# Optimization experiments

Hardware: AMD Instinct MI355X
Metric: run time of the kernel (lower is better)

Reference implementation:

```python
import jax, jax.numpy as jnp
import numpy as np

N_NODES = 100000
N_EDGES = 1600000
IN_C = 128
HID = 128
LAT = 64
N_LAYERS = 3
N_GRAPHS = 1000


def setup_inputs() -> dict:
    key = jax.random.key(0)
    ks = jax.random.split(key, 16)
    x = jax.random.normal(ks[0], (N_NODES, IN_C), dtype=jnp.float32)
    edge_index = jax.random.randint(ks[1], (2, N_EDGES), 0, N_NODES, dtype=jnp.int64)
    batch = jnp.sort(jax.random.randint(ks[2], (N_NODES,), 0, N_GRAPHS, dtype=jnp.int64))
    s = 1.0 / np.sqrt(HID)
    # per-layer GIN MLP params (in_c == hidden for all layers since IN_C == HID)
    W1 = jax.random.normal(ks[3], (N_LAYERS, IN_C, HID), dtype=jnp.float32) * s
    b1 = jnp.zeros((N_LAYERS, HID), dtype=jnp.float32)
    W2 = jax.random.normal(ks[4], (N_LAYERS, HID, HID), dtype=jnp.float32) * s
    b2 = jnp.zeros((N_LAYERS, HID), dtype=jnp.float32)
    W_mu = jax.random.normal(ks[5], (HID, LAT), dtype=jnp.float32) * s
    b_mu = jnp.zeros((LAT,), dtype=jnp.float32)
    W_lv = jax.random.normal(ks[6], (HID, LAT), dtype=jnp.float32) * s
    b_lv = jnp.zeros((LAT,), dtype=jnp.float32)
    return {"x": x, "edge_index": edge_index, "batch": batch,
            "W1": W1, "b1": b1, "W2": W2, "b2": b2,
            "W_mu": W_mu, "b_mu": b_mu, "W_lv": W_lv, "b_lv": b_lv}


def reference(x, edge_index, batch, W1, b1, W2, b2, W_mu, b_mu, W_lv, b_lv):
    src, dst = edge_index[0], edge_index[1]
    h = x
    for i in range(N_LAYERS):
        # GINConv (eps=0): h' = MLP(h + sum_{j in N(i)} h_j); scatter-add over edges
        agg = h + jax.ops.segment_sum(h[src], dst, num_segments=N_NODES)
        h = jax.nn.relu(agg @ W1[i] + b1[i])
        h = jax.nn.relu(h @ W2[i] + b2[i])
        h = jax.nn.relu(h)  # extra ReLU in forward after conv (idempotent here)
    # global_add_pool: segment-sum nodes into graphs
    g = jax.ops.segment_sum(h, batch, num_segments=N_GRAPHS)  # [G, HID]
    mu = g @ W_mu + b_mu
    logvar = g @ W_lv + b_lv
    return (mu, logvar)
```

## Files before the change

kernel.cpp:

```cpp
#include <hip/hip_runtime.h>

#define N_NODES 100000
#define N_EDGES 1600000
#define HID 128
#define LAT 64
#define N_LAYERS 3
#define N_GRAPHS 1000
#define CAP 64
#define NBIN 391
#define MAXBIN 4608
#define ACHUNK 8192
#define ABLOCKS ((N_EDGES + ACHUNK - 1) / ACHUNK)

typedef short bf16x8 __attribute__((ext_vector_type(8)));
typedef float f32x4 __attribute__((ext_vector_type(4)));

__device__ __forceinline__ float bf2f(unsigned short h) {
    union { unsigned int u; float f; } c;
    c.u = ((unsigned int)h) << 16;
    return c.f;
}
__device__ __forceinline__ unsigned short f2bf(float f) {
    union { float f; unsigned int u; } c;
    c.f = f;
    unsigned int u = c.u;
    return (unsigned short)((u + 0x7fffu + ((u >> 16) & 1u)) >> 16);
}
__device__ __forceinline__ unsigned int pack2(float a, float b) {
    return (unsigned int)f2bf(a) | ((unsigned int)f2bf(b) << 16);
}
__device__ __forceinline__ void addrow(float* acc, uint4 w) {
    acc[0] += bf2f((unsigned short)w.x); acc[1] += bf2f((unsigned short)(w.x >> 16));
    acc[2] += bf2f((unsigned short)w.y); acc[3] += bf2f((unsigned short)(w.y >> 16));
    acc[4] += bf2f((unsigned short)w.z); acc[5] += bf2f((unsigned short)(w.z >> 16));
    acc[6] += bf2f((unsigned short)w.w); acc[7] += bf2f((unsigned short)(w.w >> 16));
}

__global__ __launch_bounds__(256) void cvt_x_kernel(const float* __restrict__ x,
                                                    unsigned short* __restrict__ xb, int n4) {
    int i = blockIdx.x * 256 + threadIdx.x;
    if (i >= n4) return;
    float4 v = ((const float4*)x)[i];
    ((uint2*)xb)[i] = make_uint2(pack2(v.x, v.y), pack2(v.z, v.w));
}

__global__ __launch_bounds__(256) void wt_kernel(const float* __restrict__ W1,
                                                 const float* __restrict__ W2,
                                                 unsigned short* __restrict__ Wt) {
    int m = blockIdx.x;
    const float* W = ((m & 1) ? W2 : W1) + (size_t)(m >> 1) * HID * HID;
    unsigned short* D = Wt + (size_t)m * HID * HID;
    for (int idx = threadIdx.x; idx < HID * HID; idx += 256) {
        int n = idx >> 7, k = idx & 127;
        D[n * HID + k] = f2bf(W[k * HID + n]);
    }
}

__global__ __launch_bounds__(256) void binA_kernel(const int* __restrict__ ei,
                                                   int* __restrict__ gcnt,
                                                   unsigned int* __restrict__ ebin) {
    __shared__ unsigned int scount[NBIN];
    __shared__ unsigned int sfill[NBIN];
    int t = threadIdx.x;
    int base = blockIdx.x * ACHUNK;
    int n = N_EDGES - base;
    if (n > ACHUNK) n = ACHUNK;
    for (int i = t; i < NBIN; i += 256) scount[i] = 0u;
    __syncthreads();
    for (int i = t; i < n; i += 256) {
        int d = ei[N_EDGES + base + i];
        atomicAdd(&scount[d >> 8], 1u);
    }
    __syncthreads();
    for (int b = t; b < NBIN; b += 256) {
        unsigned int c = scount[b];
        sfill[b] = c ? (unsigned int)atomicAdd(&gcnt[b], (int)c) : 0u;
    }
    __syncthreads();
    for (int i = t; i < n; i += 256) {
        int s = ei[base + i];
        int d = ei[N_EDGES + base + i];
        int b = d >> 8;
        unsigned int pos = atomicAdd(&sfill[b], 1u);
        ebin[(size_t)b * MAXBIN + pos] = ((unsigned int)(d & 255) << 24) | (unsigned int)s;
    }
}

__global__ __launch_bounds__(256) void binB_kernel(const unsigned int* __restrict__ ebin,
                                                   const int* __restrict__ gcnt,
                                                   int* __restrict__ cnt,
                                                   int* __restrict__ csr) {
    __shared__ int scnt[256];
    int b = blockIdx.x;
    int t = threadIdx.x;
    scnt[t] = 0;
    __syncthreads();
    int n0 = b << 8;
    int c = gcnt[b];
    const unsigned int* src = ebin + (size_t)b * MAXBIN;
    for (int i = t; i < c; i += 256) {
        unsigned int e = src[i];
        int dl = (int)(e >> 24);
        int slot = atomicAdd(&scnt[dl], 1);
        csr[(size_t)(n0 + dl) * CAP + slot] = (int)(e & 0xFFFFFFu);
    }
    __syncthreads();
    int node = n0 + t;
    if (node < N_NODES) cnt[node] = scnt[t];
}

__global__ __launch_bounds__(256) void gather_kernel(const unsigned short* __restrict__ h,
                                                     const int* __restrict__ cnt,
                                                     const int* __restrict__ csr,
                                                     unsigned short* __restrict__ agg) {
    int t = threadIdx.x;
    int node = blockIdx.x * 16 + (t >> 4);
    int q = t & 15;
    if (node >= N_NODES) return;
    const int* nl = csr + (size_t)node * CAP;
    int deg = cnt[node];
    float acc[8] = {0.f, 0.f, 0.f, 0.f, 0.f, 0.f, 0.f, 0.f};
    addrow(acc, *(const uint4*)(h + (size_t)node * HID + q * 8));
    int e = 0;
    for (; e + 8 <= deg; e += 8) {
        int s0 = nl[e], s1 = nl[e + 1], s2 = nl[e + 2], s3 = nl[e + 3];
        int s4 = nl[e + 4], s5 = nl[e + 5], s6 = nl[e + 6], s7 = nl[e + 7];
        uint4 w0 = *(const uint4*)(h + (size_t)s0 * HID + q * 8);
        uint4 w1 = *(const uint4*)(h + (size_t)s1 * HID + q * 8);
        uint4 w2 = *(const uint4*)(h + (size_t)s2 * HID + q * 8);
        uint4 w3 = *(const uint4*)(h + (size_t)s3 * HID + q * 8);
        uint4 w4 = *(const uint4*)(h + (size_t)s4 * HID + q * 8);
        uint4 w5 = *(const uint4*)(h + (size_t)s5 * HID + q * 8);
        uint4 w6 = *(const uint4*)(h + (size_t)s6 * HID + q * 8);
        uint4 w7 = *(const uint4*)(h + (size_t)s7 * HID + q * 8);
        addrow(acc, w0); addrow(acc, w1); addrow(acc, w2); addrow(acc, w3);
        addrow(acc, w4); addrow(acc, w5); addrow(acc, w6); addrow(acc, w7);
    }
    for (; e + 4 <= deg; e += 4) {
        int s0 = nl[e], s1 = nl[e + 1], s2 = nl[e + 2], s3 = nl[e + 3];
        uint4 w0 = *(const uint4*)(h + (size_t)s0 * HID + q * 8);
        uint4 w1 = *(const uint4*)(h + (size_t)s1 * HID + q * 8);
        uint4 w2 = *(const uint4*)(h + (size_t)s2 * HID + q * 8);
        uint4 w3 = *(const uint4*)(h + (size_t)s3 * HID + q * 8);
        addrow(acc, w0); addrow(acc, w1); addrow(acc, w2); addrow(acc, w3);
    }
    for (; e < deg; ++e) {
        addrow(acc, *(const uint4*)(h + (size_t)nl[e] * HID + q * 8));
    }
    uint4 o;
    o.x = pack2(acc[0], acc[1]);
    o.y = pack2(acc[2], acc[3]);
    o.z = pack2(acc[4], acc[5]);
    o.w = pack2(acc[6], acc[7]);
    *(uint4*)(agg + (size_t)node * HID + q * 8) = o;
}

__global__ __launch_bounds__(256) void mlp_kernel(const unsigned short* __restrict__ A,
                                                  const unsigned short* __restrict__ W1t,
                                                  const float* __restrict__ b1,
                                                  const unsigned short* __restrict__ W2t,
                                                  const float* __restrict__ b2,
                                                  unsigned short* __restrict__ out) {
    __shared__ unsigned short sA[64][136];
    __shared__ unsigned short sW[128][40];
    __shared__ float sb[128];
    const int t = threadIdx.x;
    const int w = t >> 6;
    const int l = t & 63;
    const int lm = l & 15;
    const int quad = l >> 4;
    const int row0 = blockIdx.x * 64;

    for (int idx = t; idx < 1024; idx += 256) {
        int r = idx >> 4, c = idx & 15;
        int grow = row0 + r;
        uint4 v = make_uint4(0u, 0u, 0u, 0u);
        if (grow < N_NODES) v = *(const uint4*)(A + (size_t)grow * HID + c * 8);
        *(uint4*)&sA[r][c * 8] = v;
    }

    const unsigned short* Wt[2] = {W1t, W2t};
    const float* bias[2] = {b1, b2};

    for (int p = 0; p < 2; ++p) {
        if (t < 128) sb[t] = bias[p][t];
        f32x4 acc[8];
#pragma unroll
        for (int nt = 0; nt < 8; ++nt) acc[nt] = (f32x4){0.f, 0.f, 0.f, 0.f};

        for (int kc = 0; kc < 4; ++kc) {
            __syncthreads();
            for (int idx = t; idx < 512; idx += 256) {
                int n = idx >> 2, kq = idx & 3;
                *(uint4*)&sW[n][kq * 8] =
                    *(const uint4*)(Wt[p] + (size_t)n * HID + kc * 32 + kq * 8);
            }
            __syncthreads();
            bf16x8 a = *(const bf16x8*)&sA[w * 16 + lm][kc * 32 + quad * 8];
#pragma unroll
            for (int nt = 0; nt < 8; ++nt) {
                bf16x8 b = *(const bf16x8*)&sW[nt * 16 + lm][quad * 8];
                acc[nt] = __builtin_amdgcn_mfma_f32_16x16x32_bf16(a, b, acc[nt], 0, 0, 0);
            }
        }
        __syncthreads();
#pragma unroll
        for (int nt = 0; nt < 8; ++nt) {
            float bv = sb[nt * 16 + lm];
#pragma unroll
            for (int r = 0; r < 4; ++r) {
                int m = w * 16 + quad * 4 + r;
                float val = fmaxf(acc[nt][r] + bv, 0.f);
                sA[m][nt * 16 + lm] = f2bf(val);
            }
        }
        __syncthreads();
    }
    for (int idx = t; idx < 1024; idx += 256) {
        int r = idx >> 4, c = idx & 15;
        int grow = row0 + r;
        if (grow < N_NODES)
            *(uint4*)(out + (size_t)grow * HID + c * 8) = *(const uint4*)&sA[r][c * 8];
    }
}

__global__ __launch_bounds__(256) void pool_kernel(const unsigned short* __restrict__ h,
                                                   const int* __restrict__ batch,
                                                   float* __restrict__ g) {
    const int S = 16;
    int t = threadIdx.x;
    int grp = t >> 4;
    int q = t & 15;
    int n0 = (blockIdx.x * 16 + grp) * S;
    if (n0 >= N_NODES) return;
    int n1 = n0 + S;
    if (n1 > N_NODES) n1 = N_NODES;
    int cur = batch[n0];
    float acc[8] = {0.f, 0.f, 0.f, 0.f, 0.f, 0.f, 0.f, 0.f};
    for (int n = n0; n < n1; ++n) {
        int b = batch[n];
        if (b != cur) {
            float* gp = g + (size_t)cur * HID + q * 8;
#pragma unroll
            for (int i = 0; i < 8; ++i) { atomicAdd(gp + i, acc[i]); acc[i] = 0.f; }
            cur = b;
        }
        addrow(acc, *(const uint4*)(h + (size_t)n * HID + q * 8));
    }
    float* gp = g + (size_t)cur * HID + q * 8;
#pragma unroll
    for (int i = 0; i < 8; ++i) atomicAdd(gp + i, acc[i]);
}

__global__ __launch_bounds__(128) void head_kernel(const float* __restrict__ g,
                                                   const float* __restrict__ Wmu,
                                                   const float* __restrict__ bmu,
                                                   const float* __restrict__ Wlv,
                                                   const float* __restrict__ blv,
                                                   float* __restrict__ out) {
    __shared__ float sg[HID];
    int gi = blockIdx.x;
    sg[threadIdx.x] = g[(size_t)gi * HID + threadIdx.x];
    __syncthreads();
    int j = threadIdx.x & 63;
    bool is_lv = threadIdx.x >= 64;
    const float* W = is_lv ? Wlv : Wmu;
    float acc = is_lv ? blv[j] : bmu[j];
    for (int k = 0; k < HID; ++k) acc = fmaf(sg[k], W[k * LAT + j], acc);
    out[(is_lv ? (size_t)N_GRAPHS * LAT : 0) + (size_t)gi * LAT + j] = acc;
}

extern "C" void kernel_launch(void* const* d_in, const int* in_sizes, int n_in,
                              void* d_out, int out_size, void* d_ws, size_t ws_size,
                              hipStream_t stream) {
    const float* x     = (const float*)d_in[0];
    const int*   ei    = (const int*)d_in[1];
    const int*   batch = (const int*)d_in[2];
    const float* W1    = (const float*)d_in[3];
    const float* b1    = (const float*)d_in[4];
    const float* W2    = (const float*)d_in[5];
    const float* b2    = (const float*)d_in[6];
    const float* Wmu   = (const float*)d_in[7];
    const float* bmu   = (const float*)d_in[8];
    const float* Wlv   = (const float*)d_in[9];
    const float* blv   = (const float*)d_in[10];
    float* out = (float*)d_out;

    float* g = (float*)d_ws;
    unsigned short* xb   = (unsigned short*)(g + (size_t)N_GRAPHS * HID);
    unsigned short* agg  = xb + (size_t)N_NODES * HID;
    unsigned short* hbuf = agg + (size_t)N_NODES * HID;
    unsigned short* Wt   = hbuf + (size_t)N_NODES * HID;
    int* cnt  = (int*)(Wt + (size_t)6 * HID * HID);
    int* gcnt = cnt + N_NODES;
    int* csr  = gcnt + NBIN + 1;
    unsigned int* ebin = (unsigned int*)(csr + (size_t)N_NODES * CAP);

    hipMemsetAsync(gcnt, 0, (size_t)NBIN * sizeof(int), stream);
    binA_kernel<<<ABLOCKS, 256, 0, stream>>>(ei, gcnt, ebin);
    binB_kernel<<<NBIN, 256, 0, stream>>>(ebin, gcnt, cnt, csr);

    cvt_x_kernel<<<(N_NODES * HID / 4 + 255) / 256, 256, 0, stream>>>(x, xb,
                                                                      N_NODES * HID / 4);
    wt_kernel<<<6, 256, 0, stream>>>(W1, W2, Wt);

    const unsigned short* hcur = xb;
    for (int i = 0; i < N_LAYERS; ++i) {
        gather_kernel<<<(N_NODES + 15) / 16, 256, 0, stream>>>(hcur, cnt, csr, agg);
        mlp_kernel<<<(N_NODES + 63) / 64, 256, 0, stream>>>(
            agg, Wt + (size_t)(2 * i) * HID * HID, b1 + (size_t)i * HID,
            Wt + (size_t)(2 * i + 1) * HID * HID, b2 + (size_t)i * HID, hbuf);
        hcur = hbuf;
    }
    hipMemsetAsync(g, 0, (size_t)N_GRAPHS * HID * sizeof(float), stream);
    pool_kernel<<<(N_NODES + 255) / 256, 256, 0, stream>>>(hcur, batch, g);
    head_kernel<<<N_GRAPHS, 128, 0, stream>>>(g, Wmu, bmu, Wlv, blv, out);
}
```

Baseline: 466.4 us.

## Remove shared-memory weight staging and barriers from MLP kernel

The fused two-layer MLP kernel no longer stages weight tiles and the input tile in LDS behind repeated block-wide barriers. Each wave now loads its 16 A rows and the bf16 weight fragments directly from global memory, keeping the intermediate activation in a per-wave LDS slice. Only one barrier remains, before the coalesced output store. This trades barrier stalls and LDS traffic for redundant global or L2 weight reads by every wave, plus a possible missing wave-level sync between the LDS writes and reads of the intermediate.

```diff
diff --git a/kernel.cpp b/kernel.cpp
--- a/kernel.cpp
+++ b/kernel.cpp
@@ -161,66 +161,64 @@
                                                   const unsigned short* __restrict__ W2t,
                                                   const float* __restrict__ b2,
                                                   unsigned short* __restrict__ out) {
-    __shared__ unsigned short sA[64][136];
-    __shared__ unsigned short sW[128][40];
-    __shared__ float sb[128];
+    __shared__ unsigned short sH[4][16][136];
     const int t = threadIdx.x;
     const int w = t >> 6;
     const int l = t & 63;
     const int lm = l & 15;
     const int quad = l >> 4;
-    const int row0 = blockIdx.x * 64;
-
+    const int row0 = blockIdx.x * 64 + w * 16;
+
+    int arow = row0 + lm;
+    if (arow >= N_NODES) arow = N_NODES - 1;
+    const unsigned short* Arow = A + (size_t)arow * HID;
+    f32x4 acc[8];
+#pragma unroll
+    for (int nt = 0; nt < 8; ++nt) acc[nt] = (f32x4){0.f, 0.f, 0.f, 0.f};
+#pragma unroll
+    for (int kc = 0; kc < 4; ++kc) {
+        bf16x8 a = *(const bf16x8*)(Arow + kc * 32 + quad * 8);
+#pragma unroll
+        for (int nt = 0; nt < 8; ++nt) {
+            bf16x8 b = *(const bf16x8*)(W1t + (size_t)(nt * 16 + lm) * HID + kc * 32 + quad * 8);
+            acc[nt] = __builtin_amdgcn_mfma_f32_16x16x32_bf16(a, b, acc[nt], 0, 0, 0);
+        }
+    }
+#pragma unroll
+    for (int nt = 0; nt < 8; ++nt) {
+        float bv = b1[nt * 16 + lm];
+#pragma unroll
+        for (int r = 0; r < 4; ++r) {
+            sH[w][quad * 4 + r][nt * 16 + lm] = f2bf(fmaxf(acc[nt][r] + bv, 0.f));
+        }
+    }
+
+    f32x4 acc2[8];
+#pragma unroll
+    for (int nt = 0; nt < 8; ++nt) acc2[nt] = (f32x4){0.f, 0.f, 0.f, 0.f};
+#pragma unroll
+    for (int kc = 0; kc < 4; ++kc) {
+        bf16x8 a = *(const bf16x8*)&sH[w][lm][kc * 32 + quad * 8];
+#pragma unroll
+        for (int nt = 0; nt < 8; ++nt) {
+            bf16x8 b = *(const bf16x8*)(W2t + (size_t)(nt * 16 + lm) * HID + kc * 32 + quad * 8);
+            acc2[nt] = __builtin_amdgcn_mfma_f32_16x16x32_bf16(a, b, acc2[nt], 0, 0, 0);
+        }
+    }
+#pragma unroll
+    for (int nt = 0; nt < 8; ++nt) {
+        float bv = b2[nt * 16 + lm];
+#pragma unroll
+        for (int r = 0; r < 4; ++r) {
+            sH[w][quad * 4 + r][nt * 16 + lm] = f2bf(fmaxf(acc2[nt][r] + bv, 0.f));
+        }
+    }
+    __syncthreads();
     for (int idx = t; idx < 1024; idx += 256) {
         int r = idx >> 4, c = idx & 15;
-        int grow = row0 + r;
-        uint4 v = make_uint4(0u, 0u, 0u, 0u);
-        if (grow < N_NODES) v = *(const uint4*)(A + (size_t)grow * HID + c * 8);
-        *(uint4*)&sA[r][c * 8] = v;
-    }
-
-    const unsigned short* Wt[2] = {W1t, W2t};
-    const float* bias[2] = {b1, b2};
-
-    for (int p = 0; p < 2; ++p) {
-        if (t < 128) sb[t] = bias[p][t];
-        f32x4 acc[8];
-#pragma unroll
-        for (int nt = 0; nt < 8; ++nt) acc[nt] = (f32x4){0.f, 0.f, 0.f, 0.f};
-
-        for (int kc = 0; kc < 4; ++kc) {
-            __syncthreads();
-            for (int idx = t; idx < 512; idx += 256) {
-                int n = idx >> 2, kq = idx & 3;
-                *(uint4*)&sW[n][kq * 8] =
-                    *(const uint4*)(Wt[p] + (size_t)n * HID + kc * 32 + kq * 8);
-            }
-            __syncthreads();
-            bf16x8 a = *(const bf16x8*)&sA[w * 16 + lm][kc * 32 + quad * 8];
-#pragma unroll
-            for (int nt = 0; nt < 8; ++nt) {
-                bf16x8 b = *(const bf16x8*)&sW[nt * 16 + lm][quad * 8];
-                acc[nt] = __builtin_amdgcn_mfma_f32_16x16x32_bf16(a, b, acc[nt], 0, 0, 0);
-            }
-        }
-        __syncthreads();
-#pragma unroll
-        for (int nt = 0; nt < 8; ++nt) {
-            float bv = sb[nt * 16 + lm];
-#pragma unroll
-            for (int r = 0; r < 4; ++r) {
-                int m = w * 16 + quad * 4 + r;
-                float val = fmaxf(acc[nt][r] + bv, 0.f);
-                sA[m][nt * 16 + lm] = f2bf(val);
-            }
-        }
-        __syncthreads();
-    }
-    for (int idx = t; idx < 1024; idx += 256) {
-        int r = idx >> 4, c = idx & 15;
-        int grow = row0 + r;
+        int grow = blockIdx.x * 64 + r;
         if (grow < N_NODES)
-            *(uint4*)(out + (size_t)grow * HID + c * 8) = *(const uint4*)&sA[r][c * 8];
+            *(uint4*)(out + (size_t)grow * HID + c * 8) = *(const uint4*)&sH[r >> 4][r & 15][c * 8];
     }
 }
 
```

After: 565.9 us. 21.3% more time.

## Fuse pooling into last MLP, merge prep kernels and memsets

Applied to the files above, without the earlier changes.

Global add pooling now runs inside the final-layer MLP kernel, reading the MLP output from shared memory and issuing segmented atomic adds. This removes the separate pool kernel and the write and re-read of the last hidden state. The input-conversion and weight-transpose kernels are merged into one launch, and the two memsets are combined into one contiguous memset by moving the bin counters next to the pool buffer. The cost is more atomics per graph, since each 64-row tile flushes its own partial sums.

```diff
diff --git a/kernel.cpp b/kernel.cpp
--- a/kernel.cpp
+++ b/kernel.cpp
@@ -11,6 +11,7 @@
 #define MAXBIN 4608
 #define ACHUNK 8192
 #define ABLOCKS ((N_EDGES + ACHUNK - 1) / ACHUNK)
+#define CVT_BLOCKS (N_NODES * HID / 4 / 256)
 
 typedef short bf16x8 __attribute__((ext_vector_type(8)));
 typedef float f32x4 __attribute__((ext_vector_type(4)));
@@ -36,24 +37,25 @@
     acc[6] += bf2f((unsigned short)w.w); acc[7] += bf2f((unsigned short)(w.w >> 16));
 }
 
-__global__ __launch_bounds__(256) void cvt_x_kernel(const float* __restrict__ x,
-                                                    unsigned short* __restrict__ xb, int n4) {
-    int i = blockIdx.x * 256 + threadIdx.x;
-    if (i >= n4) return;
+__global__ __launch_bounds__(256) void prep_kernel(const float* __restrict__ x,
+                                                   unsigned short* __restrict__ xb,
+                                                   const float* __restrict__ W1,
+                                                   const float* __restrict__ W2,
+                                                   unsigned short* __restrict__ Wt) {
+    int blk = blockIdx.x;
+    if (blk < 6) {
+        const float* W = ((blk & 1) ? W2 : W1) + (size_t)(blk >> 1) * HID * HID;
+        unsigned short* D = Wt + (size_t)blk * HID * HID;
+        for (int idx = threadIdx.x; idx < HID * HID; idx += 256) {
+            int n = idx >> 7, k = idx & 127;
+            D[n * HID + k] = f2bf(W[k * HID + n]);
+        }
+        return;
+    }
+    int i = (blk - 6) * 256 + threadIdx.x;
+    if (i >= N_NODES * HID / 4) return;
     float4 v = ((const float4*)x)[i];
     ((uint2*)xb)[i] = make_uint2(pack2(v.x, v.y), pack2(v.z, v.w));
-}
-
-__global__ __launch_bounds__(256) void wt_kernel(const float* __restrict__ W1,
-                                                 const float* __restrict__ W2,
-                                                 unsigned short* __restrict__ Wt) {
-    int m = blockIdx.x;
-    const float* W = ((m & 1) ? W2 : W1) + (size_t)(m >> 1) * HID * HID;
-    unsigned short* D = Wt + (size_t)m * HID * HID;
-    for (int idx = threadIdx.x; idx < HID * HID; idx += 256) {
-        int n = idx >> 7, k = idx & 127;
-        D[n * HID + k] = f2bf(W[k * HID + n]);
-    }
 }
 
 __global__ __launch_bounds__(256) void binA_kernel(const int* __restrict__ ei,
@@ -160,10 +162,13 @@
                                                   const float* __restrict__ b1,
                                                   const unsigned short* __restrict__ W2t,
                                                   const float* __restrict__ b2,
-                                                  unsigned short* __restrict__ out) {
+                                                  unsigned short* __restrict__ out,
+                                                  const int* __restrict__ batch,
+                                                  float* __restrict__ gpool) {
     __shared__ unsigned short sA[64][136];
     __shared__ unsigned short sW[128][40];
     __shared__ float sb[128];
+    __shared__ int sbatch[64];
     const int t = threadIdx.x;
     const int w = t >> 6;
     const int l = t & 63;
@@ -177,6 +182,10 @@
         uint4 v = make_uint4(0u, 0u, 0u, 0u);
         if (grow < N_NODES) v = *(const uint4*)(A + (size_t)grow * HID + c * 8);
         *(uint4*)&sA[r][c * 8] = v;
+    }
+    if (gpool && t < 64) {
+        int n = row0 + t;
+        sbatch[t] = (n < N_NODES) ? batch[n] : -1;
     }
 
     const unsigned short* Wt[2] = {W1t, W2t};
@@ -216,40 +225,31 @@
         }
         __syncthreads();
     }
-    for (int idx = t; idx < 1024; idx += 256) {
-        int r = idx >> 4, c = idx & 15;
-        int grow = row0 + r;
-        if (grow < N_NODES)
-            *(uint4*)(out + (size_t)grow * HID + c * 8) = *(const uint4*)&sA[r][c * 8];
-    }
-}
-
-__global__ __launch_bounds__(256) void pool_kernel(const unsigned short* __restrict__ h,
-                                                   const int* __restrict__ batch,
-                                                   float* __restrict__ g) {
-    const int S = 16;
-    int t = threadIdx.x;
-    int grp = t >> 4;
-    int q = t & 15;
-    int n0 = (blockIdx.x * 16 + grp) * S;
-    if (n0 >= N_NODES) return;
-    int n1 = n0 + S;
-    if (n1 > N_NODES) n1 = N_NODES;
-    int cur = batch[n0];
-    float acc[8] = {0.f, 0.f, 0.f, 0.f, 0.f, 0.f, 0.f, 0.f};
-    for (int n = n0; n < n1; ++n) {
-        int b = batch[n];
-        if (b != cur) {
-            float* gp = g + (size_t)cur * HID + q * 8;
-#pragma unroll
-            for (int i = 0; i < 8; ++i) { atomicAdd(gp + i, acc[i]); acc[i] = 0.f; }
-            cur = b;
-        }
-        addrow(acc, *(const uint4*)(h + (size_t)n * HID + q * 8));
-    }
-    float* gp = g + (size_t)cur * HID + q * 8;
-#pragma unroll
-    for (int i = 0; i < 8; ++i) atomicAdd(gp + i, acc[i]);
+
+    if (!gpool) {
+        for (int idx = t; idx < 1024; idx += 256) {
+            int r = idx >> 4, c = idx & 15;
+            int grow = row0 + r;
+            if (grow < N_NODES)
+                *(uint4*)(out + (size_t)grow * HID + c * 8) = *(const uint4*)&sA[r][c * 8];
+        }
+    } else {
+        int c = t & 127;
+        int r0 = (t >> 7) * 32;
+        float acc = 0.f;
+        int cur = sbatch[r0];
+        for (int r = r0; r < r0 + 32; ++r) {
+            int b = sbatch[r];
+            if (b < 0) break;
+            if (b != cur) {
+                atomicAdd(&gpool[(size_t)cur * HID + c], acc);
+                acc = 0.f;
+                cur = b;
+            }
+            acc += bf2f(sA[r][c]);
+        }
+        if (cur >= 0) atomicAdd(&gpool[(size_t)cur * HID + c], acc);
+    }
 }
 
 __global__ __launch_bounds__(128) void head_kernel(const float* __restrict__ g,
@@ -286,33 +286,33 @@
     const float* blv   = (const float*)d_in[10];
     float* out = (float*)d_out;
 
-    float* g = (float*)d_ws;
-    unsigned short* xb   = (unsigned short*)(g + (size_t)N_GRAPHS * HID);
+    float* g  = (float*)d_ws;
+    int* gcnt = (int*)(g + (size_t)N_GRAPHS * HID);
+    unsigned short* xb   = (unsigned short*)(gcnt + NBIN + 1);
     unsigned short* agg  = xb + (size_t)N_NODES * HID;
     unsigned short* hbuf = agg + (size_t)N_NODES * HID;
     unsigned short* Wt   = hbuf + (size_t)N_NODES * HID;
-    int* cnt  = (int*)(Wt + (size_t)6 * HID * HID);
-    int* gcnt = cnt + N_NODES;
-    int* csr  = gcnt + NBIN + 1;
+    int* cnt = (int*)(Wt + (size_t)6 * HID * HID);
+    int* csr = cnt + N_NODES;
     unsigned int* ebin = (unsigned int*)(csr + (size_t)N_NODES * CAP);
 
-    hipMemsetAsync(gcnt, 0, (size_t)NBIN * sizeof(int), stream);
+    hipMemsetAsync(g, 0, (size_t)N_GRAPHS * HID * sizeof(float) + (NBIN + 1) * sizeof(int),
+                   stream);
+
     binA_kernel<<<ABLOCKS, 256, 0, stream>>>(ei, gcnt, ebin);
     binB_kernel<<<NBIN, 256, 0, stream>>>(ebin, gcnt, cnt, csr);
 
-    cvt_x_kernel<<<(N_NODES * HID / 4 + 255) / 256, 256, 0, stream>>>(x, xb,
-                                                                      N_NODES * HID / 4);
-    wt_kernel<<<6, 256, 0, stream>>>(W1, W2, Wt);
+    prep_kernel<<<CVT_BLOCKS + 6, 256, 0, stream>>>(x, xb, W1, W2, Wt);
 
     const unsigned short* hcur = xb;
     for (int i = 0; i < N_LAYERS; ++i) {
+        bool last = (i == N_LAYERS - 1);
         gather_kernel<<<(N_NODES + 15) / 16, 256, 0, stream>>>(hcur, cnt, csr, agg);
         mlp_kernel<<<(N_NODES + 63) / 64, 256, 0, stream>>>(
             agg, Wt + (size_t)(2 * i) * HID * HID, b1 + (size_t)i * HID,
-            Wt + (size_t)(2 * i + 1) * HID * HID, b2 + (size_t)i * HID, hbuf);
+            Wt + (size_t)(2 * i + 1) * HID * HID, b2 + (size_t)i * HID, hbuf,
+            batch, last ? g : nullptr);
         hcur = hbuf;
     }
-    hipMemsetAsync(g, 0, (size_t)N_GRAPHS * HID * sizeof(float), stream);
-    pool_kernel<<<(N_NODES + 255) / 256, 256, 0, stream>>>(hcur, batch, g);
     head_kernel<<<N_GRAPHS, 128, 0, stream>>>(g, Wmu, bmu, Wlv, blv, out);
 }
```

Result: slower. 490.8 us (+5.2%).
